# Optimization experiments

Hardware: AMD Instinct MI355X
Metric: run time of the kernel (lower is better)

Reference implementation:

```python
import jax, jax.numpy as jnp
import numpy as np

N_HEADS = 16
TOPK = 32
TEMPERATURE = 1.0
LN_EPS = 1e-5
COS_EPS = 1e-8


def setup_inputs() -> dict:
    key = jax.random.key(0)
    ks = jax.random.split(key, 10)
    B, N, M, D = 4, 512, 32768, 1024  # D == query_dim == memory_dim == output_dim
    s = 1.0 / np.sqrt(D)
    return {
        "query_states": jax.random.normal(ks[0], (B, N, D), jnp.float32),
        "memory_keys": jax.random.normal(ks[1], (M, D), jnp.float32),
        "memory_values": jax.random.normal(ks[2], (M, D), jnp.float32),
        "Wq": jax.random.normal(ks[3], (D, D), jnp.float32) * s,  # torch Linear weight [out,in]
        "Wk": jax.random.normal(ks[4], (D, D), jnp.float32) * s,
        "Wv": jax.random.normal(ks[5], (D, D), jnp.float32) * s,
        "Wo": jax.random.normal(ks[6], (D, D), jnp.float32) * s,
        "bo": jnp.zeros((D,), jnp.float32),
        "gamma": jnp.ones((D,), jnp.float32),
        "beta": jnp.zeros((D,), jnp.float32),
    }


def reference(query_states, memory_keys, memory_values, Wq, Wk, Wv, Wo, bo, gamma, beta):
    B, N, _ = query_states.shape
    M, D = memory_keys.shape  # memory_dim
    out_dim = Wq.shape[0]
    H = N_HEADS
    hd = out_dim // H
    K = min(TOPK, M)

    # --- per-position top-k selection (training path, vectorized) ---
    # query_for_sim is q_proj(x).mean(-1) broadcast to a constant vector of size D,
    # so cosine_similarity(q_pos, mk) = qm * sum(mk) / max(|qm|*sqrt(D)*||mk||, eps)
    q_full = jnp.einsum('bnd,od->bno', query_states, Wq)  # [B,N,out_dim]
    qm = q_full.mean(axis=-1)                              # [B,N]
    sum_mk = memory_keys.sum(axis=-1)                      # [M]
    norm_mk = jnp.linalg.norm(memory_keys, axis=-1)        # [M]
    sqrtD = jnp.sqrt(jnp.asarray(D, query_states.dtype))
    num = qm[..., None] * sum_mk                           # [B,N,M]
    den = jnp.maximum(jnp.abs(qm)[..., None] * sqrtD * norm_mk, COS_EPS)
    sims = num / den                                       # [B,N,M]
    _, sel_idx = jax.lax.top_k(sims, K)                    # [B,N,K]
    sel_keys = memory_keys[sel_idx]                        # [B,N,K,D]
    sel_vals = memory_values[sel_idx]                      # [B,N,K,D]

    # --- multi-head cross-attention over selected slots ---
    q = q_full.reshape(B, N, H, hd)                                   # [B,N,H,hd]
    k = jnp.einsum('bnkd,od->bnko', sel_keys, Wk).reshape(B, N, K, H, hd)
    v = jnp.einsum('bnkd,od->bnko', sel_vals, Wv).reshape(B, N, K, H, hd)
    scores = jnp.einsum('bnhd,bnkhd->bnhk', q, k) / (jnp.sqrt(jnp.asarray(hd, q.dtype)) * TEMPERATURE)
    attn = jax.nn.softmax(scores, axis=-1)                             # [B,N,H,K]
    ctx = jnp.einsum('bnhk,bnkhd->bnhd', attn, v).reshape(B, N, out_dim)
    out = jnp.einsum('bno,po->bnp', ctx, Wo) + bo
    mu = out.mean(axis=-1, keepdims=True)
    var = out.var(axis=-1, keepdims=True)
    out = (out - mu) / jnp.sqrt(var + LN_EPS) * gamma + beta
    avg_attn = attn.mean(axis=2)                                       # [B,N,K]
    return out, avg_attn, sel_idx
```

## Files before the change

kernel.cpp:

```cpp
#include <hip/hip_runtime.h>

#define BTOK   2048
#define DDIM   1024
#define MKEYS  32768
#define NHEAD  16
#define HDIM   64
#define KSEL   32

#define WS_QFULL 0
#define WS_CTX   (BTOK * DDIM)
#define WS_S     (WS_CTX + BTOK * DDIM)
#define WS_S2    (WS_S + MKEYS)
#define WS_QM    (WS_S2 + MKEYS)
#define WS_KP    (WS_QM + BTOK)
#define WS_VP    (WS_KP + 64 * DDIM)
#define WS_IDX   (WS_VP + 64 * DDIM)
#define WS_RAW   WS_QFULL

#define OUT_AVG  (BTOK * DDIM)
#define OUT_IDX  (OUT_AVG + BTOK * KSEL)

__global__ __launch_bounds__(256) void reduce_keys(const float* __restrict__ mk,
                                                   float* __restrict__ s,
                                                   float* __restrict__ s2) {
    const int w = threadIdx.x >> 6, l = threadIdx.x & 63;
    const int row = blockIdx.x * 4 + w;
    const float* r = mk + (size_t)row * DDIM;
    float sum = 0.f, sq = 0.f;
#pragma unroll
    for (int i = 0; i < 4; ++i) {
        float4 v = *(const float4*)(r + i * 256 + l * 4);
        sum += v.x + v.y + v.z + v.w;
        sq  += v.x * v.x + v.y * v.y + v.z * v.z + v.w * v.w;
    }
#pragma unroll
    for (int off = 32; off; off >>= 1) {
        sum += __shfl_down(sum, off);
        sq  += __shfl_down(sq, off);
    }
    if (l == 0) {
        float val = sum / sqrtf(sq);
        s[row]  = val;
        s2[row] = -val;
    }
}

__global__ __launch_bounds__(1024) void topk_radix(const float* __restrict__ sarr,
                                                   int* __restrict__ idx_out) {
    const float* s = sarr + blockIdx.x * MKEYS;
    int* out = idx_out + blockIdx.x * KSEL;
    const int t = threadIdx.x;

    __shared__ int   hist[4096];
    __shared__ int   csum[64];
    __shared__ int   binB_s;
    __shared__ int   ccnt;
    __shared__ float cval[1024];
    __shared__ int   cidx[1024];

    for (int i = t; i < 4096; i += 1024) hist[i] = 0;
    if (t == 0) ccnt = 0;
    __syncthreads();

    for (int j = 0; j < 32; ++j) {
        unsigned u = __float_as_uint(s[t + j * 1024]);
        unsigned k = u ^ (unsigned)(((int)u >> 31) | (int)0x80000000);
        atomicAdd(&hist[k >> 20], 1);
    }
    __syncthreads();

    if (t < 64) {
        int acc = 0;
        for (int j = 0; j < 64; ++j) acc += hist[t * 64 + j];
        csum[t] = acc;
    }
    __syncthreads();
    if (t == 0) {
        int acc = 0, cb = 63;
        for (; cb > 0; --cb) {
            if (acc + csum[cb] >= KSEL) break;
            acc += csum[cb];
        }
        int b = cb * 64 + 63;
        for (; b > cb * 64; --b) {
            if (acc + hist[b] >= KSEL) break;
            acc += hist[b];
        }
        binB_s = b;
    }
    __syncthreads();
    const unsigned binB = (unsigned)binB_s;

    for (int j = 0; j < 32; ++j) {
        const int ii = t + j * 1024;
        float v = s[ii];
        unsigned u = __float_as_uint(v);
        unsigned k = u ^ (unsigned)(((int)u >> 31) | (int)0x80000000);
        if ((k >> 20) >= binB) {
            int p = atomicAdd(&ccnt, 1);
            if (p < 1024) { cval[p] = v; cidx[p] = ii; }
        }
    }
    __syncthreads();

    const int n = min(ccnt, 1024);
    if (t < 64) {
        for (int iter = 0; iter < KSEL; ++iter) {
            float bv = -INFINITY; int bi = 0x7fffffff; int bs = -1;
            for (int j = t; j < n; j += 64) {
                float v = cval[j]; int ii = cidx[j];
                if (v > bv || (v == bv && ii < bi)) { bv = v; bi = ii; bs = j; }
            }
#pragma unroll
            for (int off = 32; off; off >>= 1) {
                float ov = __shfl_down(bv, off);
                int   oi = __shfl_down(bi, off);
                int   os = __shfl_down(bs, off);
                if (ov > bv || (ov == bv && oi < bi)) { bv = ov; bi = oi; bs = os; }
            }
            bs = __shfl(bs, 0);
            if (t == 0) {
                out[iter] = bi;
                cval[bs] = -INFINITY;
            }
        }
    }
}

__device__ __forceinline__ void gemm_body(const float* __restrict__ A,
                                          const float* __restrict__ B,
                                          float* __restrict__ C,
                                          int N, int Kdim,
                                          const int* __restrict__ gidx,
                                          int m0, int n0) {
    __shared__ float As[2][16][68];
    __shared__ float Bs[2][16][68];
    const int tid = threadIdx.x;
    const int tx = tid & 15, ty = tid >> 4;
    const int lrow = tid >> 2;
    const int lk = (tid & 3) * 4;
    const int arow = gidx ? gidx[m0 + lrow] : (m0 + lrow);
    const float* aptr = A + (size_t)arow * Kdim + lk;
    const float* bptr = B + (size_t)(n0 + lrow) * Kdim + lk;

    float4 av = *(const float4*)(aptr);
    float4 bv = *(const float4*)(bptr);
    As[0][lk + 0][lrow] = av.x; As[0][lk + 1][lrow] = av.y;
    As[0][lk + 2][lrow] = av.z; As[0][lk + 3][lrow] = av.w;
    Bs[0][lk + 0][lrow] = bv.x; Bs[0][lk + 1][lrow] = bv.y;
    Bs[0][lk + 2][lrow] = bv.z; Bs[0][lk + 3][lrow] = bv.w;
    __syncthreads();

    float acc[4][4] = {};
    const int nt = Kdim >> 4;
    int cb = 0;
    for (int tk = 0; tk < nt; ++tk) {
        float4 av2, bv2;
        const bool more = (tk + 1 < nt);
        if (more) {
            av2 = *(const float4*)(aptr + (tk + 1) * 16);
            bv2 = *(const float4*)(bptr + (tk + 1) * 16);
        }
#pragma unroll
        for (int kk = 0; kk < 16; ++kk) {
            float a[4], b[4];
#pragma unroll
            for (int i = 0; i < 4; ++i) a[i] = As[cb][kk][ty * 4 + i];
#pragma unroll
            for (int j = 0; j < 4; ++j) b[j] = Bs[cb][kk][tx * 4 + j];
#pragma unroll
            for (int i = 0; i < 4; ++i)
#pragma unroll
                for (int j = 0; j < 4; ++j) acc[i][j] += a[i] * b[j];
        }
        if (more) {
            const int nb = cb ^ 1;
            As[nb][lk + 0][lrow] = av2.x; As[nb][lk + 1][lrow] = av2.y;
            As[nb][lk + 2][lrow] = av2.z; As[nb][lk + 3][lrow] = av2.w;
            Bs[nb][lk + 0][lrow] = bv2.x; Bs[nb][lk + 1][lrow] = bv2.y;
            Bs[nb][lk + 2][lrow] = bv2.z; Bs[nb][lk + 3][lrow] = bv2.w;
        }
        __syncthreads();
        cb ^= 1;
    }

    float* cp = C + (size_t)(m0 + ty * 4) * N + n0 + tx * 4;
#pragma unroll
    for (int i = 0; i < 4; ++i) {
        float4 o = make_float4(acc[i][0], acc[i][1], acc[i][2], acc[i][3]);
        *(float4*)(cp + (size_t)i * N) = o;
    }
}

__global__ __launch_bounds__(256) void gemm_nt(const float* __restrict__ A,
                                               const float* __restrict__ B,
                                               float* __restrict__ C,
                                               int N, int Kdim,
                                               const int* __restrict__ gidx) {
    gemm_body(A, B, C, N, Kdim, gidx, blockIdx.y * 64, blockIdx.x * 64);
}

__global__ __launch_bounds__(256) void gemm_kv(const float* __restrict__ mk,
                                               const float* __restrict__ mv,
                                               const float* __restrict__ Wk,
                                               const float* __restrict__ Wv,
                                               float* __restrict__ kp,
                                               float* __restrict__ vp,
                                               const int* __restrict__ gidx) {
    const int which = blockIdx.y;
    const float* A = which ? mv : mk;
    const float* B = which ? Wv : Wk;
    float*       C = which ? vp : kp;
    gemm_body(A, B, C, DDIM, DDIM, gidx, 0, blockIdx.x * 64);
}

__global__ __launch_bounds__(256) void qm_kernel(const float* __restrict__ q_full,
                                                 float* __restrict__ qm) {
    const int w = threadIdx.x >> 6, l = threadIdx.x & 63;
    const int row = blockIdx.x * 4 + w;
    const float* r = q_full + (size_t)row * DDIM;
    float s = 0.f;
#pragma unroll
    for (int i = 0; i < 4; ++i) {
        float4 v = *(const float4*)(r + i * 256 + l * 4);
        s += v.x + v.y + v.z + v.w;
    }
#pragma unroll
    for (int off = 32; off; off >>= 1) s += __shfl_down(s, off);
    if (l == 0) qm[row] = s * (1.f / 1024.f);
}

__global__ __launch_bounds__(256) void attention_kernel(const float* __restrict__ q_full,
                                                        const float* __restrict__ qm,
                                                        const float* __restrict__ kp,
                                                        const float* __restrict__ vp,
                                                        const int* __restrict__ idx_list,
                                                        float* __restrict__ ctx,
                                                        float* __restrict__ out) {
    const int bn = blockIdx.x;
    const int t = threadIdx.x;
    __shared__ float qs[DDIM];
    __shared__ float sc[NHEAD][KSEL + 1];
    __shared__ int selbase_s;

    *(float4*)(qs + t * 4) = *(const float4*)(q_full + (size_t)bn * DDIM + t * 4);
    if (t == 0) selbase_s = (qm[bn] > 0.0f) ? 0 : KSEL;
    __syncthreads();
    const int selbase = selbase_s;

#pragma unroll
    for (int p = 0; p < 2; ++p) {
        const int pair = t + p * 256;
        const int h = pair >> 5, k = pair & 31;
        const float* kr = kp + (size_t)(selbase + k) * DDIM + h * HDIM;
        const float* qr = qs + h * HDIM;
        float acc = 0.f;
#pragma unroll
        for (int i = 0; i < 16; ++i) {
            float4 kv = *(const float4*)(kr + i * 4);
            acc += qr[i * 4 + 0] * kv.x + qr[i * 4 + 1] * kv.y +
                   qr[i * 4 + 2] * kv.z + qr[i * 4 + 3] * kv.w;
        }
        sc[h][k] = acc * 0.125f;
    }
    __syncthreads();

    if (t < NHEAD) {
        float m = -INFINITY;
        for (int k = 0; k < KSEL; ++k) m = fmaxf(m, sc[t][k]);
        float ssum = 0.f;
        for (int k = 0; k < KSEL; ++k) { float e = __expf(sc[t][k] - m); sc[t][k] = e; ssum += e; }
        float inv = 1.f / ssum;
        for (int k = 0; k < KSEL; ++k) sc[t][k] *= inv;
    }
    __syncthreads();

#pragma unroll
    for (int c = 0; c < 4; ++c) {
        const int o = c * 256 + t;
        const int h = o >> 6;
        float acc = 0.f;
        for (int k = 0; k < KSEL; ++k)
            acc += sc[h][k] * vp[(size_t)(selbase + k) * DDIM + o];
        ctx[(size_t)bn * DDIM + o] = acc;
    }

    if (t < KSEL) {
        float a = 0.f;
#pragma unroll
        for (int h = 0; h < NHEAD; ++h) a += sc[h][t];
        out[OUT_AVG + bn * KSEL + t] = a * (1.f / 16.f);
        out[OUT_IDX + bn * KSEL + t] = (float)idx_list[selbase + t];
    }
}

__global__ __launch_bounds__(256) void ln_kernel(const float* __restrict__ raw,
                                                 const float* __restrict__ bo,
                                                 const float* __restrict__ gamma,
                                                 const float* __restrict__ beta,
                                                 float* __restrict__ out) {
    const int row = blockIdx.x;
    const int t = threadIdx.x;
    float4 v = *(const float4*)(raw + (size_t)row * DDIM + t * 4);
    float4 b = *(const float4*)(bo + t * 4);
    v.x += b.x; v.y += b.y; v.z += b.z; v.w += b.w;
    float s  = v.x + v.y + v.z + v.w;
    float ss = v.x * v.x + v.y * v.y + v.z * v.z + v.w * v.w;
#pragma unroll
    for (int off = 32; off; off >>= 1) {
        s  += __shfl_down(s, off);
        ss += __shfl_down(ss, off);
    }
    __shared__ float rs[4], rss[4];
    const int w = t >> 6, l = t & 63;
    if (l == 0) { rs[w] = s; rss[w] = ss; }
    __syncthreads();
    if (t == 0) {
        rs[0]  = rs[0] + rs[1] + rs[2] + rs[3];
        rss[0] = rss[0] + rss[1] + rss[2] + rss[3];
    }
    __syncthreads();
    const float mu  = rs[0] * (1.f / 1024.f);
    const float var = rss[0] * (1.f / 1024.f) - mu * mu;
    const float rstd = rsqrtf(var + 1e-5f);
    float4 g  = *(const float4*)(gamma + t * 4);
    float4 be = *(const float4*)(beta + t * 4);
    float4 o;
    o.x = (v.x - mu) * rstd * g.x + be.x;
    o.y = (v.y - mu) * rstd * g.y + be.y;
    o.z = (v.z - mu) * rstd * g.z + be.z;
    o.w = (v.w - mu) * rstd * g.w + be.w;
    *(float4*)(out + (size_t)row * DDIM + t * 4) = o;
}

extern "C" void kernel_launch(void* const* d_in, const int* in_sizes, int n_in,
                              void* d_out, int out_size, void* d_ws, size_t ws_size,
                              hipStream_t stream) {
    const float* x     = (const float*)d_in[0];
    const float* mk    = (const float*)d_in[1];
    const float* mv    = (const float*)d_in[2];
    const float* Wq    = (const float*)d_in[3];
    const float* Wk    = (const float*)d_in[4];
    const float* Wv    = (const float*)d_in[5];
    const float* Wo    = (const float*)d_in[6];
    const float* bo    = (const float*)d_in[7];
    const float* gamma = (const float*)d_in[8];
    const float* beta  = (const float*)d_in[9];

    float* ws  = (float*)d_ws;
    float* out = (float*)d_out;

    float* q_full = ws + WS_QFULL;
    float* ctx    = ws + WS_CTX;
    float* sarr   = ws + WS_S;
    float* qm     = ws + WS_QM;
    float* kp     = ws + WS_KP;
    float* vp     = ws + WS_VP;
    int*   idx    = (int*)(ws + WS_IDX);
    float* raw    = ws + WS_RAW;

    hipLaunchKernelGGL(reduce_keys, dim3(MKEYS / 4), dim3(256), 0, stream, mk, sarr, sarr + MKEYS);
    hipLaunchKernelGGL(gemm_nt, dim3(16, 32), dim3(256), 0, stream, x, Wq, q_full, DDIM, DDIM, (const int*)nullptr);
    hipLaunchKernelGGL(qm_kernel, dim3(BTOK / 4), dim3(256), 0, stream, q_full, qm);
    hipLaunchKernelGGL(topk_radix, dim3(2), dim3(1024), 0, stream, sarr, idx);
    hipLaunchKernelGGL(gemm_kv, dim3(16, 2), dim3(256), 0, stream, mk, mv, Wk, Wv, kp, vp, idx);
    hipLaunchKernelGGL(attention_kernel, dim3(BTOK), dim3(256), 0, stream, q_full, qm, kp, vp, idx, ctx, out);
    hipLaunchKernelGGL(gemm_nt, dim3(16, 32), dim3(256), 0, stream, ctx, Wo, raw, DDIM, DDIM, (const int*)nullptr);
    hipLaunchKernelGGL(ln_kernel, dim3(BTOK), dim3(256), 0, stream, raw, bo, gamma, beta, out);
}
```

Measured before the change: 524.2 us.

## Switch projection GEMMs to bf16 MFMA and compute query mean via column-sum vector

```diff
diff --git a/kernel.cpp b/kernel.cpp
--- a/kernel.cpp
+++ b/kernel.cpp
@@ -7,42 +7,100 @@
 #define HDIM   64
 #define KSEL   32
 
+typedef __attribute__((ext_vector_type(4))) float f32x4;
+typedef __attribute__((ext_vector_type(8))) short bf16x8;
+
 #define WS_QFULL 0
-#define WS_CTX   (BTOK * DDIM)
-#define WS_S     (WS_CTX + BTOK * DDIM)
+#define WS_CTXB  (2*1024*1024)
+#define WS_S     (WS_CTXB + 1024*1024)
 #define WS_S2    (WS_S + MKEYS)
 #define WS_QM    (WS_S2 + MKEYS)
 #define WS_KP    (WS_QM + BTOK)
-#define WS_VP    (WS_KP + 64 * DDIM)
-#define WS_IDX   (WS_VP + 64 * DDIM)
+#define WS_VP    (WS_KP + 64*1024)
+#define WS_IDX   (WS_VP + 64*1024)
+#define WS_XB    (WS_IDX + 64)
+#define WS_WQB   (WS_XB + 1024*1024)
+#define WS_WKB   (WS_WQB + 512*1024)
+#define WS_WVB   (WS_WKB + 512*1024)
+#define WS_WOB   (WS_WVB + 512*1024)
+#define WS_CVEC  (WS_WOB + 512*1024)
 #define WS_RAW   WS_QFULL
 
 #define OUT_AVG  (BTOK * DDIM)
 #define OUT_IDX  (OUT_AVG + BTOK * KSEL)
 
-__global__ __launch_bounds__(256) void reduce_keys(const float* __restrict__ mk,
-                                                   float* __restrict__ s,
-                                                   float* __restrict__ s2) {
+__device__ __forceinline__ unsigned short f2bf(float f) {
+    unsigned u = __float_as_uint(f);
+    u += 0x7fffu + ((u >> 16) & 1u);
+    return (unsigned short)(u >> 16);
+}
+
+__global__ __launch_bounds__(256) void prep_kernel(
+        const float* __restrict__ mk, const float* __restrict__ x,
+        const float* __restrict__ Wq, const float* __restrict__ Wk,
+        const float* __restrict__ Wv, const float* __restrict__ Wo,
+        float* __restrict__ s, float* __restrict__ s2,
+        unsigned short* __restrict__ xb, unsigned short* __restrict__ wqb,
+        unsigned short* __restrict__ wkb, unsigned short* __restrict__ wvb,
+        unsigned short* __restrict__ wob, float* __restrict__ cvec) {
+    const int b = blockIdx.x, t = threadIdx.x;
+    if (b < 8192) {
+        const int w = t >> 6, l = t & 63;
+        const int row = b * 4 + w;
+        const float* r = mk + (size_t)row * DDIM;
+        float sum = 0.f, sq = 0.f;
+#pragma unroll
+        for (int i = 0; i < 4; ++i) {
+            float4 v = *(const float4*)(r + i * 256 + l * 4);
+            sum += v.x + v.y + v.z + v.w;
+            sq  += v.x * v.x + v.y * v.y + v.z * v.z + v.w * v.w;
+        }
+#pragma unroll
+        for (int off = 32; off; off >>= 1) {
+            sum += __shfl_down(sum, off);
+            sq  += __shfl_down(sq, off);
+        }
+        if (l == 0) {
+            float val = sum / sqrtf(sq);
+            s[row] = val; s2[row] = -val;
+        }
+    } else if (b < 14336) {
+        const float* src; unsigned short* dst; int blk;
+        if (b < 10240)      { src = x;  dst = xb;  blk = b - 8192; }
+        else if (b < 11264) { src = Wq; dst = wqb; blk = b - 10240; }
+        else if (b < 12288) { src = Wk; dst = wkb; blk = b - 11264; }
+        else if (b < 13312) { src = Wv; dst = wvb; blk = b - 12288; }
+        else                { src = Wo; dst = wob; blk = b - 13312; }
+        const size_t base = (size_t)blk * 1024 + t * 4;
+        float4 v = *(const float4*)(src + base);
+        ushort4 o;
+        o.x = f2bf(v.x); o.y = f2bf(v.y); o.z = f2bf(v.z); o.w = f2bf(v.w);
+        *(ushort4*)(dst + base) = o;
+    } else {
+        const int d = (b - 14336) * 256 + t;
+        float acc = 0.f;
+#pragma unroll 8
+        for (int o = 0; o < 1024; ++o) acc += Wq[(size_t)o * 1024 + d];
+        cvec[d] = acc * (1.f / 1024.f);
+    }
+}
+
+__global__ __launch_bounds__(256) void qm_dot(const float* __restrict__ x,
+                                              const float* __restrict__ cvec,
+                                              float* __restrict__ qm) {
     const int w = threadIdx.x >> 6, l = threadIdx.x & 63;
     const int row = blockIdx.x * 4 + w;
-    const float* r = mk + (size_t)row * DDIM;
-    float sum = 0.f, sq = 0.f;
+    const float* r = x + (size_t)row * DDIM;
+    float s = 0.f;
 #pragma unroll
     for (int i = 0; i < 4; ++i) {
         float4 v = *(const float4*)(r + i * 256 + l * 4);
-        sum += v.x + v.y + v.z + v.w;
-        sq  += v.x * v.x + v.y * v.y + v.z * v.z + v.w * v.w;
-    }
-#pragma unroll
-    for (int off = 32; off; off >>= 1) {
-        sum += __shfl_down(sum, off);
-        sq  += __shfl_down(sq, off);
-    }
-    if (l == 0) {
-        float val = sum / sqrtf(sq);
-        s[row]  = val;
-        s2[row] = -val;
-    }
+        float4 c = *(const float4*)(cvec + i * 256 + l * 4);
+        s += v.x * c.x + v.y * c.y + v.z * c.z + v.w * c.w;
+    }
+#pragma unroll
+    for (int off = 32; off; off >>= 1) s += __shfl_down(s, off);
+    if (l == 0) qm[row] = s;
 }
 
 __global__ __launch_bounds__(1024) void topk_radix(const float* __restrict__ sarr,
@@ -127,107 +185,105 @@
     }
 }
 
-__device__ __forceinline__ void gemm_body(const float* __restrict__ A,
-                                          const float* __restrict__ B,
-                                          float* __restrict__ C,
-                                          int N, int Kdim,
-                                          const int* __restrict__ gidx,
-                                          int m0, int n0) {
-    __shared__ float As[2][16][68];
-    __shared__ float Bs[2][16][68];
-    const int tid = threadIdx.x;
-    const int tx = tid & 15, ty = tid >> 4;
-    const int lrow = tid >> 2;
-    const int lk = (tid & 3) * 4;
-    const int arow = gidx ? gidx[m0 + lrow] : (m0 + lrow);
-    const float* aptr = A + (size_t)arow * Kdim + lk;
-    const float* bptr = B + (size_t)(n0 + lrow) * Kdim + lk;
-
-    float4 av = *(const float4*)(aptr);
-    float4 bv = *(const float4*)(bptr);
-    As[0][lk + 0][lrow] = av.x; As[0][lk + 1][lrow] = av.y;
-    As[0][lk + 2][lrow] = av.z; As[0][lk + 3][lrow] = av.w;
-    Bs[0][lk + 0][lrow] = bv.x; Bs[0][lk + 1][lrow] = bv.y;
-    Bs[0][lk + 2][lrow] = bv.z; Bs[0][lk + 3][lrow] = bv.w;
-    __syncthreads();
-
-    float acc[4][4] = {};
-    const int nt = Kdim >> 4;
-    int cb = 0;
-    for (int tk = 0; tk < nt; ++tk) {
-        float4 av2, bv2;
-        const bool more = (tk + 1 < nt);
-        if (more) {
-            av2 = *(const float4*)(aptr + (tk + 1) * 16);
-            bv2 = *(const float4*)(bptr + (tk + 1) * 16);
-        }
-#pragma unroll
-        for (int kk = 0; kk < 16; ++kk) {
-            float a[4], b[4];
-#pragma unroll
-            for (int i = 0; i < 4; ++i) a[i] = As[cb][kk][ty * 4 + i];
-#pragma unroll
-            for (int j = 0; j < 4; ++j) b[j] = Bs[cb][kk][tx * 4 + j];
-#pragma unroll
-            for (int i = 0; i < 4; ++i)
-#pragma unroll
-                for (int j = 0; j < 4; ++j) acc[i][j] += a[i] * b[j];
-        }
-        if (more) {
-            const int nb = cb ^ 1;
-            As[nb][lk + 0][lrow] = av2.x; As[nb][lk + 1][lrow] = av2.y;
-            As[nb][lk + 2][lrow] = av2.z; As[nb][lk + 3][lrow] = av2.w;
-            Bs[nb][lk + 0][lrow] = bv2.x; Bs[nb][lk + 1][lrow] = bv2.y;
-            Bs[nb][lk + 2][lrow] = bv2.z; Bs[nb][lk + 3][lrow] = bv2.w;
-        }
-        __syncthreads();
-        cb ^= 1;
-    }
-
-    float* cp = C + (size_t)(m0 + ty * 4) * N + n0 + tx * 4;
+__global__ __launch_bounds__(256) void gemm_mfma(const unsigned short* __restrict__ A,
+                                                 const unsigned short* __restrict__ Bm,
+                                                 float* __restrict__ C) {
+    const int lane = threadIdx.x & 63, wave = threadIdx.x >> 6;
+    const int quad = lane >> 4, l16 = lane & 15;
+    const int m0 = blockIdx.y * 128 + (wave >> 1) * 64;
+    const int n0 = blockIdx.x * 128 + (wave & 1) * 64;
+    const unsigned short* ap = A + (size_t)(m0 + l16) * DDIM + quad * 8;
+    const unsigned short* bp = Bm + (size_t)(n0 + l16) * DDIM + quad * 8;
+
+    const f32x4 fzero = {0.f, 0.f, 0.f, 0.f};
+    f32x4 acc[4][4];
+#pragma unroll
+    for (int i = 0; i < 4; ++i)
+#pragma unroll
+        for (int j = 0; j < 4; ++j) acc[i][j] = fzero;
+
+    for (int k0 = 0; k0 < DDIM; k0 += 32) {
+        bf16x8 af[4], bfr[4];
+#pragma unroll
+        for (int i = 0; i < 4; ++i)
+            af[i] = *(const bf16x8*)(ap + (size_t)i * 16 * DDIM + k0);
+#pragma unroll
+        for (int j = 0; j < 4; ++j)
+            bfr[j] = *(const bf16x8*)(bp + (size_t)j * 16 * DDIM + k0);
+#pragma unroll
+        for (int i = 0; i < 4; ++i)
+#pragma unroll
+            for (int j = 0; j < 4; ++j)
+                acc[i][j] = __builtin_amdgcn_mfma_f32_16x16x32_bf16(af[i], bfr[j], acc[i][j], 0, 0, 0);
+    }
 #pragma unroll
     for (int i = 0; i < 4; ++i) {
-        float4 o = make_float4(acc[i][0], acc[i][1], acc[i][2], acc[i][3]);
-        *(float4*)(cp + (size_t)i * N) = o;
-    }
-}
-
-__global__ __launch_bounds__(256) void gemm_nt(const float* __restrict__ A,
-                                               const float* __restrict__ B,
-                                               float* __restrict__ C,
-                                               int N, int Kdim,
-                                               const int* __restrict__ gidx) {
-    gemm_body(A, B, C, N, Kdim, gidx, blockIdx.y * 64, blockIdx.x * 64);
-}
-
-__global__ __launch_bounds__(256) void gemm_kv(const float* __restrict__ mk,
-                                               const float* __restrict__ mv,
-                                               const float* __restrict__ Wk,
-                                               const float* __restrict__ Wv,
-                                               float* __restrict__ kp,
-                                               float* __restrict__ vp,
-                                               const int* __restrict__ gidx) {
-    const int which = blockIdx.y;
-    const float* A = which ? mv : mk;
-    const float* B = which ? Wv : Wk;
-    float*       C = which ? vp : kp;
-    gemm_body(A, B, C, DDIM, DDIM, gidx, 0, blockIdx.x * 64);
-}
-
-__global__ __launch_bounds__(256) void qm_kernel(const float* __restrict__ q_full,
-                                                 float* __restrict__ qm) {
-    const int w = threadIdx.x >> 6, l = threadIdx.x & 63;
-    const int row = blockIdx.x * 4 + w;
-    const float* r = q_full + (size_t)row * DDIM;
-    float s = 0.f;
+        const int row0 = m0 + i * 16 + quad * 4;
+#pragma unroll
+        for (int j = 0; j < 4; ++j) {
+            const int col = n0 + j * 16 + l16;
+#pragma unroll
+            for (int r = 0; r < 4; ++r)
+                C[(size_t)(row0 + r) * DDIM + col] = acc[i][j][r];
+        }
+    }
+}
+
+__global__ __launch_bounds__(256) void gemm_kv_mfma(
+        const float* __restrict__ mk, const float* __restrict__ mv,
+        const unsigned short* __restrict__ wkb, const unsigned short* __restrict__ wvb,
+        float* __restrict__ kp, float* __restrict__ vp,
+        const int* __restrict__ gidx) {
+    const float* A = blockIdx.y ? mv : mk;
+    const unsigned short* Bm = blockIdx.y ? wvb : wkb;
+    float* C = blockIdx.y ? vp : kp;
+    const int lane = threadIdx.x & 63, wave = threadIdx.x >> 6;
+    const int quad = lane >> 4, l16 = lane & 15;
+    const int n0 = blockIdx.x * 256 + wave * 64;
+
+    size_t arow[4];
+#pragma unroll
+    for (int i = 0; i < 4; ++i) arow[i] = (size_t)gidx[i * 16 + l16] * DDIM;
+
+    const f32x4 fzero = {0.f, 0.f, 0.f, 0.f};
+    f32x4 acc[4][4];
+#pragma unroll
+    for (int i = 0; i < 4; ++i)
+#pragma unroll
+        for (int j = 0; j < 4; ++j) acc[i][j] = fzero;
+
+    for (int k0 = 0; k0 < DDIM; k0 += 32) {
+        bf16x8 af[4], bfr[4];
+#pragma unroll
+        for (int i = 0; i < 4; ++i) {
+            const float* p = A + arow[i] + k0 + quad * 8;
+            float4 v0 = *(const float4*)(p);
+            float4 v1 = *(const float4*)(p + 4);
+            af[i][0] = (short)f2bf(v0.x); af[i][1] = (short)f2bf(v0.y);
+            af[i][2] = (short)f2bf(v0.z); af[i][3] = (short)f2bf(v0.w);
+            af[i][4] = (short)f2bf(v1.x); af[i][5] = (short)f2bf(v1.y);
+            af[i][6] = (short)f2bf(v1.z); af[i][7] = (short)f2bf(v1.w);
+        }
+#pragma unroll
+        for (int j = 0; j < 4; ++j)
+            bfr[j] = *(const bf16x8*)(Bm + (size_t)(n0 + j * 16 + l16) * DDIM + k0 + quad * 8);
+#pragma unroll
+        for (int i = 0; i < 4; ++i)
+#pragma unroll
+            for (int j = 0; j < 4; ++j)
+                acc[i][j] = __builtin_amdgcn_mfma_f32_16x16x32_bf16(af[i], bfr[j], acc[i][j], 0, 0, 0);
+    }
 #pragma unroll
     for (int i = 0; i < 4; ++i) {
-        float4 v = *(const float4*)(r + i * 256 + l * 4);
-        s += v.x + v.y + v.z + v.w;
-    }
-#pragma unroll
-    for (int off = 32; off; off >>= 1) s += __shfl_down(s, off);
-    if (l == 0) qm[row] = s * (1.f / 1024.f);
+        const int row0 = i * 16 + quad * 4;
+#pragma unroll
+        for (int j = 0; j < 4; ++j) {
+            const int col = n0 + j * 16 + l16;
+#pragma unroll
+            for (int r = 0; r < 4; ++r)
+                C[(size_t)(row0 + r) * DDIM + col] = acc[i][j][r];
+        }
+    }
 }
 
 __global__ __launch_bounds__(256) void attention_kernel(const float* __restrict__ q_full,
@@ -235,7 +291,7 @@
                                                         const float* __restrict__ kp,
                                                         const float* __restrict__ vp,
                                                         const int* __restrict__ idx_list,
-                                                        float* __restrict__ ctx,
+                                                        unsigned short* __restrict__ ctxb,
                                                         float* __restrict__ out) {
     const int bn = blockIdx.x;
     const int t = threadIdx.x;
@@ -282,7 +338,7 @@
         float acc = 0.f;
         for (int k = 0; k < KSEL; ++k)
             acc += sc[h][k] * vp[(size_t)(selbase + k) * DDIM + o];
-        ctx[(size_t)bn * DDIM + o] = acc;
+        ctxb[(size_t)bn * DDIM + o] = f2bf(acc);
     }
 
     if (t < KSEL) {
@@ -350,21 +406,29 @@
     float* ws  = (float*)d_ws;
     float* out = (float*)d_out;
 
-    float* q_full = ws + WS_QFULL;
-    float* ctx    = ws + WS_CTX;
-    float* sarr   = ws + WS_S;
-    float* qm     = ws + WS_QM;
-    float* kp     = ws + WS_KP;
-    float* vp     = ws + WS_VP;
-    int*   idx    = (int*)(ws + WS_IDX);
-    float* raw    = ws + WS_RAW;
-
-    hipLaunchKernelGGL(reduce_keys, dim3(MKEYS / 4), dim3(256), 0, stream, mk, sarr, sarr + MKEYS);
-    hipLaunchKernelGGL(gemm_nt, dim3(16, 32), dim3(256), 0, stream, x, Wq, q_full, DDIM, DDIM, (const int*)nullptr);
-    hipLaunchKernelGGL(qm_kernel, dim3(BTOK / 4), dim3(256), 0, stream, q_full, qm);
+    float* q_full          = ws + WS_QFULL;
+    unsigned short* ctxb   = (unsigned short*)(ws + WS_CTXB);
+    float* sarr            = ws + WS_S;
+    float* qm              = ws + WS_QM;
+    float* kp              = ws + WS_KP;
+    float* vp              = ws + WS_VP;
+    int*   idx             = (int*)(ws + WS_IDX);
+    unsigned short* xb     = (unsigned short*)(ws + WS_XB);
+    unsigned short* wqb    = (unsigned short*)(ws + WS_WQB);
+    unsigned short* wkb    = (unsigned short*)(ws + WS_WKB);
+    unsigned short* wvb    = (unsigned short*)(ws + WS_WVB);
+    unsigned short* wob    = (unsigned short*)(ws + WS_WOB);
+    float* cvec            = ws + WS_CVEC;
+    float* raw             = ws + WS_RAW;
+
+    hipLaunchKernelGGL(prep_kernel, dim3(14340), dim3(256), 0, stream,
+                       mk, x, Wq, Wk, Wv, Wo, sarr, sarr + MKEYS,
+                       xb, wqb, wkb, wvb, wob, cvec);
+    hipLaunchKernelGGL(qm_dot, dim3(BTOK / 4), dim3(256), 0, stream, x, cvec, qm);
     hipLaunchKernelGGL(topk_radix, dim3(2), dim3(1024), 0, stream, sarr, idx);
-    hipLaunchKernelGGL(gemm_kv, dim3(16, 2), dim3(256), 0, stream, mk, mv, Wk, Wv, kp, vp, idx);
-    hipLaunchKernelGGL(attention_kernel, dim3(BTOK), dim3(256), 0, stream, q_full, qm, kp, vp, idx, ctx, out);
-    hipLaunchKernelGGL(gemm_nt, dim3(16, 32), dim3(256), 0, stream, ctx, Wo, raw, DDIM, DDIM, (const int*)nullptr);
+    hipLaunchKernelGGL(gemm_mfma, dim3(8, 16), dim3(256), 0, stream, xb, wqb, q_full);
+    hipLaunchKernelGGL(gemm_kv_mfma, dim3(4, 2), dim3(256), 0, stream, mk, mv, wkb, wvb, kp, vp, idx);
+    hipLaunchKernelGGL(attention_kernel, dim3(BTOK), dim3(256), 0, stream, q_full, qm, kp, vp, idx, ctxb, out);
+    hipLaunchKernelGGL(gemm_mfma, dim3(8, 16), dim3(256), 0, stream, ctxb, wob, raw);
     hipLaunchKernelGGL(ln_kernel, dim3(BTOK), dim3(256), 0, stream, raw, bo, gamma, beta, out);
 }
```

Measured after the change: 536.3 us. 2.3% more time.
